# Kernel optimization log

Measured on AMD Instinct MI355X. Metric: run time of the kernel, lower is better.

The kernel has to match this reference:

```python
import jax, jax.numpy as jnp
import numpy as np

B, T, C = 2, 2048, 1024
NH, NKV, HD, NG = 16, 8, 64, 8   # heads, kv heads, head_dim, global heads
NG_KV = NG * NKV // NH           # global kv heads = 4
VE_CH = 32                       # ve_gate input channels
WIN = 1024                       # local sliding-window (left) size


def setup_inputs() -> dict:
    key = jax.random.key(0)
    ks = jax.random.split(key, 8)
    x = jax.random.normal(ks[0], (B, T, C), jnp.float32)
    ve = jax.random.normal(ks[1], (B, T, NKV * HD), jnp.float32)
    # true rotary tables over half the head dim
    half = HD // 2
    inv_freq = 1.0 / (10000.0 ** (np.arange(half, dtype=np.float64) / half))
    ang = np.arange(T, dtype=np.float64)[:, None] * inv_freq[None, :]
    cos = jnp.asarray(np.cos(ang), jnp.float32)[None, :, None, :]  # [1,T,1,32]
    sin = jnp.asarray(np.sin(ang), jnp.float32)[None, :, None, :]
    s = C ** -0.5
    Wq = jax.random.normal(ks[2], (C, NH * HD), jnp.float32) * s
    Wk = jax.random.normal(ks[3], (C, NKV * HD), jnp.float32) * s
    Wv = jax.random.normal(ks[4], (C, NKV * HD), jnp.float32) * s
    Wproj = jax.random.normal(ks[5], (C, C), jnp.float32) * s
    Wg = jax.random.normal(ks[6], (VE_CH, NKV), jnp.float32) * (VE_CH ** -0.5)
    return dict(x=x, ve=ve, cos=cos, sin=sin, Wq=Wq, Wk=Wk, Wv=Wv,
                Wproj=Wproj, Wg=Wg, window=WIN)


def _rope(x, cos, sin):
    d = x.shape[-1] // 2
    x1, x2 = x[..., :d], x[..., d:]
    return jnp.concatenate([x1 * cos + x2 * sin, -x1 * sin + x2 * cos], axis=-1)


def _rms_norm(x):
    eps = jnp.asarray(jnp.finfo(x.dtype).eps, x.dtype)
    return x * jax.lax.rsqrt(jnp.mean(x * x, axis=-1, keepdims=True) + eps)


def _gqa_attn(q, k, v, left_window):
    # q: [B,T,Hq,D]; k,v: [B,T,Hk,D]; GQA with g = Hq//Hk queries per kv head.
    b, t, hq, d = q.shape
    hk = k.shape[2]
    g = hq // hk
    qg = q.reshape(b, t, hk, g, d)
    scores = jnp.einsum('bqhgd,bkhd->bhgqk', qg, k) * (d ** -0.5)
    i = jnp.arange(t)[:, None]
    j = jnp.arange(t)[None, :]
    if left_window < 0:
        mask = j <= i                       # full causal
    else:
        mask = (j <= i) & ((i - j) <= left_window)  # causal sliding window
    scores = jnp.where(mask, scores, jnp.asarray(-1e30, scores.dtype))
    p = jax.nn.softmax(scores, axis=-1)
    out = jnp.einsum('bhgqk,bkhd->bqhgd', p, v)
    return out.reshape(b, t, hq, d)


def reference(x, ve, cos, sin, Wq, Wk, Wv, Wproj, Wg, window):
    b, t, c = x.shape
    q = (x @ Wq).reshape(b, t, NH, HD)
    k = (x @ Wk).reshape(b, t, NKV, HD)
    v = (x @ Wv).reshape(b, t, NKV, HD)
    # value-embedding gating: gate = 2*sigmoid(Linear(x[..., :32])) per kv head
    gate = 2.0 * jax.nn.sigmoid(x[..., :VE_CH] @ Wg)       # [B,T,NKV]
    v = v + gate[..., None] * ve.reshape(b, t, NKV, HD)
    # inline RoPE then RMSNorm on q and k
    q = _rms_norm(_rope(q, cos, sin))
    k = _rms_norm(_rope(k, cos, sin))
    # split global (full causal) vs local (windowed) head groups
    y_global = _gqa_attn(q[:, :, :NG], k[:, :, :NG_KV], v[:, :, :NG_KV], -1)
    y_local = _gqa_attn(q[:, :, NG:], k[:, :, NG_KV:], v[:, :, NG_KV:], window)
    y = jnp.concatenate([y_global, y_local], axis=2).reshape(b, t, c)
    return y @ Wproj
```

## Files before the change

kernel.cpp:

```cpp
#include <hip/hip_runtime.h>
#include <hip/hip_bf16.h>
#include <math.h>

typedef __bf16 bf16x8 __attribute__((ext_vector_type(8)));
typedef __bf16 bf16x4 __attribute__((ext_vector_type(4)));
typedef float  f32x4  __attribute__((ext_vector_type(4)));

#define MFMA16(a, b, c) __builtin_amdgcn_mfma_f32_16x16x32_bf16((a), (b), (c), 0, 0, 0)

__device__ __forceinline__ void gload16(const void* g, void* lds) {
    __builtin_amdgcn_global_load_lds(
        (const __attribute__((address_space(1))) uint32_t*)g,
        (__attribute__((address_space(3))) uint32_t*)lds, 16, 0, 0);
}

__global__ __launch_bounds__(256)
void prep2_kernel(const float* __restrict__ x, __bf16* __restrict__ xb,
                  const float* __restrict__ Wq, const float* __restrict__ Wk,
                  const float* __restrict__ Wv, const float* __restrict__ Wproj,
                  __bf16* __restrict__ wqkvt, __bf16* __restrict__ wprojt) {
    const int bx = blockIdx.x;
    const int tid = threadIdx.x;
    if (bx < 4096) {
        int i = bx * 256 + tid;
        float4 v = reinterpret_cast<const float4*>(x)[i];
        bf16x4 o = { (__bf16)v.x, (__bf16)v.y, (__bf16)v.z, (__bf16)v.w };
        *reinterpret_cast<bf16x4*>(xb + (size_t)i * 4) = o;
        return;
    }
    __shared__ __bf16 Ts[64 * 72];
    const int idx = bx - 4096;
    const int z = idx >> 8;
    const float* W = (z == 0) ? Wq : (z == 1) ? Wk : (z == 2) ? Wv : Wproj;
    __bf16* dst = (z == 3) ? wprojt : wqkvt;
    const int N = (z == 1 || z == 2) ? 512 : 1024;
    const int nt_off = (z == 1) ? 1024 : (z == 2) ? 1536 : 0;
    const int n0 = (idx & 15) * 64, k0 = ((idx >> 4) & 15) * 64;
    if (n0 >= N) return;
    {
        int r = tid >> 2;
        int c0 = (tid & 3) * 16;
        const float4* s4 = reinterpret_cast<const float4*>(
            W + (size_t)(k0 + r) * N + n0 + c0);
        float val[16];
        #pragma unroll
        for (int q = 0; q < 4; ++q) {
            float4 v = s4[q];
            val[q * 4 + 0] = v.x; val[q * 4 + 1] = v.y;
            val[q * 4 + 2] = v.z; val[q * 4 + 3] = v.w;
        }
        #pragma unroll
        for (int j = 0; j < 16; ++j) Ts[(c0 + j) * 72 + r] = (__bf16)val[j];
    }
    __syncthreads();
    {
        int n = tid >> 2, kg = (tid & 3) * 16;
        __bf16* out = dst + (size_t)(nt_off + n0 + n) * 1024 + k0 + kg;
        bf16x8 t0 = *reinterpret_cast<const bf16x8*>(&Ts[n * 72 + kg]);
        bf16x8 t1 = *reinterpret_cast<const bf16x8*>(&Ts[n * 72 + kg + 8]);
        *reinterpret_cast<bf16x8*>(out) = t0;
        *reinterpret_cast<bf16x8*>(out + 8) = t1;
    }
}

template <typename OutT>
__global__ __launch_bounds__(256)
void gemm_bf16(const __bf16* __restrict__ A, const __bf16* __restrict__ Bt,
               OutT* __restrict__ C, int M, int N, int K) {
    __shared__ __align__(16) __bf16 As[128 * 64];
    __shared__ __align__(16) __bf16 Bs[128 * 64];
    const int tid = threadIdx.x;
    const int lane = tid & 63, w = tid >> 6;
    const int wr = w >> 1, wc = w & 1;
    const int nwg = gridDim.x * gridDim.y;
    const int id = blockIdx.y * gridDim.x + blockIdx.x;
    const int nid = (id & 7) * (nwg >> 3) + (id >> 3);
    const int bxs = nid % gridDim.x, bys = nid / gridDim.x;
    const int bm = bys * 128, bn = bxs * 128;
    const int lhi = lane >> 4, llo = lane & 15;
    const int gsrc = (lane & 7) ^ ((lane >> 3) & 7);

    f32x4 acc[4][4] = {};

    for (int k0 = 0; k0 < K; k0 += 64) {
        __syncthreads();
        const __bf16* Ab = A + (size_t)bm * K + k0;
        const __bf16* Bb = Bt + (size_t)bn * K + k0;
        #pragma unroll
        for (int rr = 0; rr < 4; ++rr) {
            int c = rr * 4 + w;
            int r = c * 8 + (lane >> 3);
            gload16(Ab + (size_t)r * K + gsrc * 8, (char*)As + c * 1024);
            gload16(Bb + (size_t)r * K + gsrc * 8, (char*)Bs + c * 1024);
        }
        __syncthreads();

        #pragma unroll
        for (int ks = 0; ks < 2; ++ks) {
            bf16x8 af[4], bfr[4];
            int g = ks * 4 + lhi;
            #pragma unroll
            for (int i = 0; i < 4; ++i) {
                int ra = wr * 64 + i * 16 + llo;
                af[i] = *reinterpret_cast<const bf16x8*>(
                    (const char*)As + ra * 128 + ((g ^ (ra & 7)) << 4));
                int rb = wc * 64 + i * 16 + llo;
                bfr[i] = *reinterpret_cast<const bf16x8*>(
                    (const char*)Bs + rb * 128 + ((g ^ (rb & 7)) << 4));
            }
            #pragma unroll
            for (int i = 0; i < 4; ++i)
                #pragma unroll
                for (int j = 0; j < 4; ++j)
                    acc[i][j] = MFMA16(af[i], bfr[j], acc[i][j]);
        }
    }

    #pragma unroll
    for (int i = 0; i < 4; ++i) {
        #pragma unroll
        for (int j = 0; j < 4; ++j) {
            int col = bn + wc * 64 + j * 16 + llo;
            #pragma unroll
            for (int r = 0; r < 4; ++r) {
                int row = bm + wr * 64 + i * 16 + lhi * 4 + r;
                C[(size_t)row * N + col] = (OutT)acc[i][j][r];
            }
        }
    }
}

__global__ __launch_bounds__(256)
void post2_kernel(__bf16* __restrict__ qkv, const float* __restrict__ x,
                  const float* __restrict__ ve, const float* __restrict__ Wg,
                  const float* __restrict__ cosb, const float* __restrict__ sinb,
                  __bf16* __restrict__ vT) {
    const int id = blockIdx.x;
    const int tid = threadIdx.x;
    if (id < 3072) {
        const int u = id >> 7;
        const int row = (id & 127) * 32 + (tid >> 3);
        const int j = tid & 7;
        const int t = row & 2047;
        const int off = (u < 16) ? u * 64 : 1024 + (u - 16) * 64;
        __bf16* p = qkv + (size_t)row * 2048 + off + j * 8;
        bf16x8 v8 = *(const bf16x8*)p;
        float v[8], pr[8];
        #pragma unroll
        for (int e = 0; e < 8; ++e) v[e] = (float)v8[e];
        #pragma unroll
        for (int e = 0; e < 8; ++e) pr[e] = __shfl_xor(v[e], 4, 64);
        const float* cp = cosb + t * 32 + (j & 3) * 8;
        const float* sp = sinb + t * 32 + (j & 3) * 8;
        float4 c0 = *(const float4*)cp, c1 = *(const float4*)(cp + 4);
        float4 s0 = *(const float4*)sp, s1 = *(const float4*)(sp + 4);
        float cs[8] = {c0.x, c0.y, c0.z, c0.w, c1.x, c1.y, c1.z, c1.w};
        float sn[8] = {s0.x, s0.y, s0.z, s0.w, s1.x, s1.y, s1.z, s1.w};
        float r[8];
        if (j < 4) {
            #pragma unroll
            for (int e = 0; e < 8; ++e) r[e] = v[e] * cs[e] + pr[e] * sn[e];
        } else {
            #pragma unroll
            for (int e = 0; e < 8; ++e) r[e] = v[e] * cs[e] - pr[e] * sn[e];
        }
        float s = 0.f;
        #pragma unroll
        for (int e = 0; e < 8; ++e) s = fmaf(r[e], r[e], s);
        s += __shfl_xor(s, 1, 64);
        s += __shfl_xor(s, 2, 64);
        s += __shfl_xor(s, 4, 64);
        float scale = rsqrtf(s * (1.0f / 64.0f) + 1.1920929e-07f);
        if (u < 16) scale *= 0.18033688011116012f;
        bf16x8 o;
        #pragma unroll
        for (int e = 0; e < 8; ++e) o[e] = (__bf16)(r[e] * scale);
        *(bf16x8*)p = o;
    } else {
        __shared__ __bf16 Ts[64 * 72];
        const int rem = id - 3072;
        const int ch = rem & 63;
        const int h = rem >> 6;
        {
            int r = tid >> 2, c0 = (tid & 3) * 16;
            int grow = ch * 64 + r;
            float gz = 0.f;
            {
                const float* xr = x + (size_t)grow * 1024 + (tid & 3) * 8;
                #pragma unroll
                for (int i = 0; i < 8; ++i)
                    gz = fmaf(xr[i], Wg[((tid & 3) * 8 + i) * 8 + h], gz);
                gz += __shfl_xor(gz, 1, 64);
                gz += __shfl_xor(gz, 2, 64);
            }
            float g = 2.0f / (1.0f + expf(-gz));
            const __bf16* vp = qkv + (size_t)grow * 2048 + 1536 + h * 64 + c0;
            const float* vep = ve + (size_t)grow * 512 + h * 64 + c0;
            bf16x8 v0 = *reinterpret_cast<const bf16x8*>(vp);
            bf16x8 v1 = *reinterpret_cast<const bf16x8*>(vp + 8);
            #pragma unroll
            for (int j = 0; j < 8; ++j) {
                Ts[(c0 + j) * 72 + r]     = (__bf16)((float)v0[j] + g * vep[j]);
                Ts[(c0 + 8 + j) * 72 + r] = (__bf16)((float)v1[j] + g * vep[8 + j]);
            }
        }
        __syncthreads();
        {
            int d = tid >> 2, t0l = (tid & 3) * 16;
            int b = ch >> 5, tloc = (ch & 31) * 64;
            __bf16* out = vT + ((size_t)((b * 8 + h) * 64 + d)) * 2048 + tloc + t0l;
            bf16x8 t0 = *reinterpret_cast<const bf16x8*>(&Ts[d * 72 + t0l]);
            bf16x8 t1 = *reinterpret_cast<const bf16x8*>(&Ts[d * 72 + t0l + 8]);
            *reinterpret_cast<bf16x8*>(out) = t0;
            *reinterpret_cast<bf16x8*>(out + 8) = t1;
        }
    }
}

__global__ __launch_bounds__(256, 6)
void attn_mfma(const __bf16* __restrict__ qkv, const __bf16* __restrict__ vT,
               __bf16* __restrict__ y, const int* __restrict__ winp) {
    __shared__ __align__(16) __bf16 Ks[64 * 64];
    __shared__ __align__(16) __bf16 VTs[64 * 64];
    __shared__ __align__(16) __bf16 Ps[4][16 * 64];

    const int bid = blockIdx.x;
    const int kvh = bid & 7;
    int tdec = bid >> 3;
    const int b = tdec & 1; tdec >>= 1;
    const int qh = tdec & 1;
    const int qt = 31 - (tdec >> 1);
    const int h = (kvh < 4) ? (kvh * 2 + qh) : (8 + (kvh - 4) * 2 + qh);
    const int q0 = qt * 64;
    const int tid = threadIdx.x, lane = tid & 63, w = tid >> 6;
    const int lhi = lane >> 4, llo = lane & 15;
    const int gsrc = (lane & 7) ^ ((lane >> 3) & 7);
    const int win = (h < 8) ? -1 : winp[0];
    const int winv = (win < 0) ? (1 << 30) : win;

    const __bf16* kbase = qkv + (size_t)(b * 2048) * 2048 + 1024 + kvh * 64;
    const __bf16* vtbase = vT + ((size_t)((b * 8 + kvh) * 64)) * 2048;

    int kts = 0;
    if (win >= 0) { int s = q0 - win; if (s > 0) kts = s >> 6; }

    const __bf16* qrow = qkv + (size_t)(b * 2048 + q0 + w * 16 + llo) * 2048
                         + h * 64 + lhi * 8;
    bf16x8 qf[2];
    qf[0] = *(const bf16x8*)(qrow);
    qf[1] = *(const bf16x8*)(qrow + 32);

    auto STAGE = [&](int ktx) {
        #pragma unroll
        for (int rr = 0; rr < 2; ++rr) {
            int c = rr * 4 + w;
            int r = c * 8 + (lane >> 3);
            gload16(kbase + (size_t)(ktx * 64 + r) * 2048 + gsrc * 8,
                    (char*)Ks + c * 1024);
            gload16(vtbase + (size_t)r * 2048 + ktx * 64 + gsrc * 8,
                    (char*)VTs + c * 1024);
        }
    };

    f32x4 oaccT[4] = {};
    float lrow = 0.f;

    const int pswz = (llo & 7) << 4;

    for (int kt = kts; kt <= qt; ++kt) {
        STAGE(kt);
        __syncthreads();

        f32x4 sacc[4] = {};
        __builtin_amdgcn_s_setprio(1);
        #pragma unroll
        for (int ks = 0; ks < 2; ++ks) {
            #pragma unroll
            for (int kj = 0; kj < 4; ++kj) {
                int rb = kj * 16 + llo;
                bf16x8 bk = *(const bf16x8*)((const char*)&Ks[0]
                    + rb * 128 + (((ks * 4 + lhi) ^ (rb & 7)) << 4));
                sacc[kj] = MFMA16(bk, qf[ks], sacc[kj]);
            }
        }
        __builtin_amdgcn_s_setprio(0);

        const bool needMask = (kt == qt) || (win >= 0 && kt * 64 < q0 + 63 - winv);

        float sv[16];
        #pragma unroll
        for (int kj = 0; kj < 4; ++kj)
            #pragma unroll
            for (int r = 0; r < 4; ++r)
                sv[kj * 4 + r] = sacc[kj][r];
        if (needMask) {
            int qrowi = q0 + w * 16 + llo;
            #pragma unroll
            for (int kj = 0; kj < 4; ++kj)
                #pragma unroll
                for (int r = 0; r < 4; ++r) {
                    int key = kt * 64 + kj * 16 + lhi * 4 + r;
                    bool ok = (key <= qrowi) && (qrowi - key <= winv);
                    if (!ok) sv[kj * 4 + r] = -__builtin_inff();
                }
        }

        float p[16];
        #pragma unroll
        for (int t = 0; t < 16; ++t)
            p[t] = __builtin_amdgcn_exp2f(sv[t]);

        #pragma unroll
        for (int kj = 0; kj < 4; ++kj) {
            bf16x4 pk = { (__bf16)p[kj * 4 + 0], (__bf16)p[kj * 4 + 1],
                          (__bf16)p[kj * 4 + 2], (__bf16)p[kj * 4 + 3] };
            *(bf16x4*)((char*)&Ps[w][0]
                + ((llo * 128 + kj * 32 + lhi * 8) ^ pswz)) = pk;
        }

        #pragma unroll
        for (int st = 8; st >= 1; st >>= 1)
            #pragma unroll
            for (int t = 0; t < st; ++t) p[t] += p[t + st];
        lrow += p[0];

        __builtin_amdgcn_s_setprio(1);
        #pragma unroll
        for (int ks = 0; ks < 2; ++ks) {
            bf16x8 ap = *(const bf16x8*)((const char*)&Ps[w][0]
                + ((llo * 128 + ks * 64 + lhi * 16) ^ pswz));
            #pragma unroll
            for (int dj = 0; dj < 4; ++dj) {
                int rv = dj * 16 + llo;
                bf16x8 bv = *(const bf16x8*)((const char*)&VTs[0]
                    + rv * 128 + (((ks * 4 + lhi) ^ (rv & 7)) << 4));
                oaccT[dj] = MFMA16(bv, ap, oaccT[dj]);
            }
        }
        __builtin_amdgcn_s_setprio(0);

        __syncthreads();
    }

    lrow += __shfl_xor(lrow, 16, 64);
    lrow += __shfl_xor(lrow, 32, 64);

    float inv = 1.0f / lrow;
    int row = b * 2048 + q0 + w * 16 + llo;
    #pragma unroll
    for (int dj = 0; dj < 4; ++dj) {
        bf16x4 o = { (__bf16)(oaccT[dj][0] * inv), (__bf16)(oaccT[dj][1] * inv),
                     (__bf16)(oaccT[dj][2] * inv), (__bf16)(oaccT[dj][3] * inv) };
        *(bf16x4*)(&y[(size_t)row * 1024 + h * 64 + dj * 16 + lhi * 4]) = o;
    }
}

extern "C" void kernel_launch(void* const* d_in, const int* in_sizes, int n_in,
                              void* d_out, int out_size, void* d_ws, size_t ws_size,
                              hipStream_t stream) {
    const float* x     = (const float*)d_in[0];
    const float* ve    = (const float*)d_in[1];
    const float* cosb  = (const float*)d_in[2];
    const float* sinb  = (const float*)d_in[3];
    const float* Wq    = (const float*)d_in[4];
    const float* Wk    = (const float*)d_in[5];
    const float* Wv    = (const float*)d_in[6];
    const float* Wproj = (const float*)d_in[7];
    const float* Wg    = (const float*)d_in[8];
    const int*   winp  = (const int*)d_in[9];

    char* ws = (char*)d_ws;
    __bf16* qkv    = (__bf16*)(ws);
    __bf16* vT     = (__bf16*)(ws + (16u << 20));
    __bf16* ybuf   = (__bf16*)(ws + (20u << 20));
    __bf16* xb     = (__bf16*)(ws + (28u << 20));
    __bf16* wqkvt  = (__bf16*)(ws + (36u << 20));
    __bf16* wprojt = (__bf16*)(ws + (40u << 20));

    prep2_kernel<<<5120, 256, 0, stream>>>(x, xb, Wq, Wk, Wv, Wproj, wqkvt, wprojt);
    gemm_bf16<__bf16><<<dim3(16, 32), 256, 0, stream>>>(xb, wqkvt, qkv, 4096, 2048, 1024);
    post2_kernel<<<3584, 256, 0, stream>>>(qkv, x, ve, Wg, cosb, sinb, vT);
    attn_mfma<<<1024, 256, 0, stream>>>(qkv, vT, ybuf, winp);
    gemm_bf16<float><<<dim3(8, 32), 256, 0, stream>>>(ybuf, wprojt, (float*)d_out, 4096, 1024, 1024);
}
```

Measured before the change: 104.9 us.

## Restructure attention into single-wave blocks handling 32 query rows

The attention kernel changes from 256-thread blocks (4 waves x 16 query rows per 64-row tile) to 64-thread single-wave blocks that each process 32 query rows across two MFMA row tiles, using a 2048-block grid. Each wave loads the full K/V tile itself and reuses the K and V fragments across both row tiles, which roughly halves the LDS staging traffic per query row. It also gives finer causal work granularity, since the last key tile now ends at a 32-row boundary. In exchange each wave does all of the tile loading, and the __syncthreads barriers now cover only one wave. Occupancy changes from 6x256-thread to 2x64-thread launch bounds, which may reduce latency hiding.

```diff
diff --git a/kernel.cpp b/kernel.cpp
--- a/kernel.cpp
+++ b/kernel.cpp
@@ -217,22 +217,23 @@
     }
 }
 
-__global__ __launch_bounds__(256, 6)
+__global__ __launch_bounds__(64, 2)
 void attn_mfma(const __bf16* __restrict__ qkv, const __bf16* __restrict__ vT,
                __bf16* __restrict__ y, const int* __restrict__ winp) {
     __shared__ __align__(16) __bf16 Ks[64 * 64];
     __shared__ __align__(16) __bf16 VTs[64 * 64];
-    __shared__ __align__(16) __bf16 Ps[4][16 * 64];
+    __shared__ __align__(16) __bf16 Ps[32 * 64];
 
     const int bid = blockIdx.x;
     const int kvh = bid & 7;
-    int tdec = bid >> 3;
-    const int b = tdec & 1; tdec >>= 1;
-    const int qh = tdec & 1;
-    const int qt = 31 - (tdec >> 1);
+    const int rest = bid >> 3;
+    const int qh = rest & 1;
+    const int u = rest >> 1;
+    const int b = u & 1;
+    const int qt32 = 63 - (u >> 1);
     const int h = (kvh < 4) ? (kvh * 2 + qh) : (8 + (kvh - 4) * 2 + qh);
-    const int q0 = qt * 64;
-    const int tid = threadIdx.x, lane = tid & 63, w = tid >> 6;
+    const int q0 = qt32 * 32;
+    const int lane = threadIdx.x;
     const int lhi = lane >> 4, llo = lane & 15;
     const int gsrc = (lane & 7) ^ ((lane >> 3) & 7);
     const int win = (h < 8) ? -1 : winp[0];
@@ -243,98 +244,107 @@
 
     int kts = 0;
     if (win >= 0) { int s = q0 - win; if (s > 0) kts = s >> 6; }
-
-    const __bf16* qrow = qkv + (size_t)(b * 2048 + q0 + w * 16 + llo) * 2048
+    const int ktlast = (q0 + 31) >> 6;
+
+    const __bf16* qrow = qkv + (size_t)(b * 2048 + q0 + llo) * 2048
                          + h * 64 + lhi * 8;
-    bf16x8 qf[2];
-    qf[0] = *(const bf16x8*)(qrow);
-    qf[1] = *(const bf16x8*)(qrow + 32);
-
-    auto STAGE = [&](int ktx) {
-        #pragma unroll
-        for (int rr = 0; rr < 2; ++rr) {
-            int c = rr * 4 + w;
-            int r = c * 8 + (lane >> 3);
-            gload16(kbase + (size_t)(ktx * 64 + r) * 2048 + gsrc * 8,
-                    (char*)Ks + c * 1024);
-            gload16(vtbase + (size_t)r * 2048 + ktx * 64 + gsrc * 8,
-                    (char*)VTs + c * 1024);
-        }
-    };
-
-    f32x4 oaccT[4] = {};
-    float lrow = 0.f;
-
+    bf16x8 qf[2][2];
+    qf[0][0] = *(const bf16x8*)(qrow);
+    qf[0][1] = *(const bf16x8*)(qrow + 32);
+    qf[1][0] = *(const bf16x8*)(qrow + 16 * 2048);
+    qf[1][1] = *(const bf16x8*)(qrow + 16 * 2048 + 32);
+
+    f32x4 oaccT[2][4] = {};
+    float lrow[2] = {0.f, 0.f};
     const int pswz = (llo & 7) << 4;
 
-    for (int kt = kts; kt <= qt; ++kt) {
-        STAGE(kt);
+    for (int kt = kts; kt <= ktlast; ++kt) {
+        #pragma unroll
+        for (int i = 0; i < 8; ++i) {
+            int r = i * 8 + (lane >> 3);
+            gload16(kbase + (size_t)(kt * 64 + r) * 2048 + gsrc * 8,
+                    (char*)Ks + i * 1024);
+            gload16(vtbase + (size_t)r * 2048 + kt * 64 + gsrc * 8,
+                    (char*)VTs + i * 1024);
+        }
         __syncthreads();
 
-        f32x4 sacc[4] = {};
+        bf16x8 bk[4][2];
+        #pragma unroll
+        for (int kj = 0; kj < 4; ++kj) {
+            int rb = kj * 16 + llo;
+            #pragma unroll
+            for (int ks = 0; ks < 2; ++ks)
+                bk[kj][ks] = *(const bf16x8*)((const char*)&Ks[0]
+                    + rb * 128 + (((ks * 4 + lhi) ^ (rb & 7)) << 4));
+        }
+        f32x4 sacc[2][4] = {};
         __builtin_amdgcn_s_setprio(1);
         #pragma unroll
+        for (int ks = 0; ks < 2; ++ks)
+            #pragma unroll
+            for (int mi = 0; mi < 2; ++mi)
+                #pragma unroll
+                for (int kj = 0; kj < 4; ++kj)
+                    sacc[mi][kj] = MFMA16(bk[kj][ks], qf[mi][ks], sacc[mi][kj]);
+        __builtin_amdgcn_s_setprio(0);
+
+        const bool needMask = (kt == ktlast) ||
+                              (win >= 0 && kt * 64 < q0 + 31 - winv);
+
+        #pragma unroll
+        for (int mi = 0; mi < 2; ++mi) {
+            float sv[16];
+            #pragma unroll
+            for (int kj = 0; kj < 4; ++kj)
+                #pragma unroll
+                for (int r = 0; r < 4; ++r)
+                    sv[kj * 4 + r] = sacc[mi][kj][r];
+            if (needMask) {
+                int qrowi = q0 + mi * 16 + llo;
+                #pragma unroll
+                for (int kj = 0; kj < 4; ++kj)
+                    #pragma unroll
+                    for (int r = 0; r < 4; ++r) {
+                        int key = kt * 64 + kj * 16 + lhi * 4 + r;
+                        bool ok = (key <= qrowi) && (qrowi - key <= winv);
+                        if (!ok) sv[kj * 4 + r] = -__builtin_inff();
+                    }
+            }
+            float p[16];
+            #pragma unroll
+            for (int t = 0; t < 16; ++t)
+                p[t] = __builtin_amdgcn_exp2f(sv[t]);
+            #pragma unroll
+            for (int kj = 0; kj < 4; ++kj) {
+                bf16x4 pk = { (__bf16)p[kj * 4 + 0], (__bf16)p[kj * 4 + 1],
+                              (__bf16)p[kj * 4 + 2], (__bf16)p[kj * 4 + 3] };
+                *(bf16x4*)((char*)&Ps[0]
+                    + (((mi * 16 + llo) * 128 + kj * 32 + lhi * 8) ^ pswz)) = pk;
+            }
+            #pragma unroll
+            for (int st = 8; st >= 1; st >>= 1)
+                #pragma unroll
+                for (int t = 0; t < st; ++t) p[t] += p[t + st];
+            lrow[mi] += p[0];
+        }
+
+        __builtin_amdgcn_s_setprio(1);
+        #pragma unroll
         for (int ks = 0; ks < 2; ++ks) {
-            #pragma unroll
-            for (int kj = 0; kj < 4; ++kj) {
-                int rb = kj * 16 + llo;
-                bf16x8 bk = *(const bf16x8*)((const char*)&Ks[0]
-                    + rb * 128 + (((ks * 4 + lhi) ^ (rb & 7)) << 4));
-                sacc[kj] = MFMA16(bk, qf[ks], sacc[kj]);
-            }
-        }
-        __builtin_amdgcn_s_setprio(0);
-
-        const bool needMask = (kt == qt) || (win >= 0 && kt * 64 < q0 + 63 - winv);
-
-        float sv[16];
-        #pragma unroll
-        for (int kj = 0; kj < 4; ++kj)
-            #pragma unroll
-            for (int r = 0; r < 4; ++r)
-                sv[kj * 4 + r] = sacc[kj][r];
-        if (needMask) {
-            int qrowi = q0 + w * 16 + llo;
-            #pragma unroll
-            for (int kj = 0; kj < 4; ++kj)
-                #pragma unroll
-                for (int r = 0; r < 4; ++r) {
-                    int key = kt * 64 + kj * 16 + lhi * 4 + r;
-                    bool ok = (key <= qrowi) && (qrowi - key <= winv);
-                    if (!ok) sv[kj * 4 + r] = -__builtin_inff();
-                }
-        }
-
-        float p[16];
-        #pragma unroll
-        for (int t = 0; t < 16; ++t)
-            p[t] = __builtin_amdgcn_exp2f(sv[t]);
-
-        #pragma unroll
-        for (int kj = 0; kj < 4; ++kj) {
-            bf16x4 pk = { (__bf16)p[kj * 4 + 0], (__bf16)p[kj * 4 + 1],
-                          (__bf16)p[kj * 4 + 2], (__bf16)p[kj * 4 + 3] };
-            *(bf16x4*)((char*)&Ps[w][0]
-                + ((llo * 128 + kj * 32 + lhi * 8) ^ pswz)) = pk;
-        }
-
-        #pragma unroll
-        for (int st = 8; st >= 1; st >>= 1)
-            #pragma unroll
-            for (int t = 0; t < st; ++t) p[t] += p[t + st];
-        lrow += p[0];
-
-        __builtin_amdgcn_s_setprio(1);
-        #pragma unroll
-        for (int ks = 0; ks < 2; ++ks) {
-            bf16x8 ap = *(const bf16x8*)((const char*)&Ps[w][0]
-                + ((llo * 128 + ks * 64 + lhi * 16) ^ pswz));
+            bf16x8 ap[2];
+            #pragma unroll
+            for (int mi = 0; mi < 2; ++mi)
+                ap[mi] = *(const bf16x8*)((const char*)&Ps[0]
+                    + (((mi * 16 + llo) * 128 + ks * 64 + lhi * 16) ^ pswz));
             #pragma unroll
             for (int dj = 0; dj < 4; ++dj) {
                 int rv = dj * 16 + llo;
                 bf16x8 bv = *(const bf16x8*)((const char*)&VTs[0]
                     + rv * 128 + (((ks * 4 + lhi) ^ (rv & 7)) << 4));
-                oaccT[dj] = MFMA16(bv, ap, oaccT[dj]);
+                #pragma unroll
+                for (int mi = 0; mi < 2; ++mi)
+                    oaccT[mi][dj] = MFMA16(bv, ap[mi], oaccT[mi][dj]);
             }
         }
         __builtin_amdgcn_s_setprio(0);
@@ -342,16 +352,24 @@
         __syncthreads();
     }
 
-    lrow += __shfl_xor(lrow, 16, 64);
-    lrow += __shfl_xor(lrow, 32, 64);
-
-    float inv = 1.0f / lrow;
-    int row = b * 2048 + q0 + w * 16 + llo;
     #pragma unroll
-    for (int dj = 0; dj < 4; ++dj) {
-        bf16x4 o = { (__bf16)(oaccT[dj][0] * inv), (__bf16)(oaccT[dj][1] * inv),
-                     (__bf16)(oaccT[dj][2] * inv), (__bf16)(oaccT[dj][3] * inv) };
-        *(bf16x4*)(&y[(size_t)row * 1024 + h * 64 + dj * 16 + lhi * 4]) = o;
+    for (int mi = 0; mi < 2; ++mi) {
+        lrow[mi] += __shfl_xor(lrow[mi], 16, 64);
+        lrow[mi] += __shfl_xor(lrow[mi], 32, 64);
+    }
+
+    #pragma unroll
+    for (int mi = 0; mi < 2; ++mi) {
+        float inv = 1.0f / lrow[mi];
+        int row = b * 2048 + q0 + mi * 16 + llo;
+        #pragma unroll
+        for (int dj = 0; dj < 4; ++dj) {
+            bf16x4 o = { (__bf16)(oaccT[mi][dj][0] * inv),
+                         (__bf16)(oaccT[mi][dj][1] * inv),
+                         (__bf16)(oaccT[mi][dj][2] * inv),
+                         (__bf16)(oaccT[mi][dj][3] * inv) };
+            *(bf16x4*)(&y[(size_t)row * 1024 + h * 64 + dj * 16 + lhi * 4]) = o;
+        }
     }
 }
 
@@ -380,6 +398,6 @@
     prep2_kernel<<<5120, 256, 0, stream>>>(x, xb, Wq, Wk, Wv, Wproj, wqkvt, wprojt);
     gemm_bf16<__bf16><<<dim3(16, 32), 256, 0, stream>>>(xb, wqkvt, qkv, 4096, 2048, 1024);
     post2_kernel<<<3584, 256, 0, stream>>>(qkv, x, ve, Wg, cosb, sinb, vT);
-    attn_mfma<<<1024, 256, 0, stream>>>(qkv, vT, ybuf, winp);
+    attn_mfma<<<2048, 64, 0, stream>>>(qkv, vT, ybuf, winp);
     gemm_bf16<float><<<dim3(8, 32), 256, 0, stream>>>(ybuf, wprojt, (float*)d_out, 4096, 1024, 1024);
 }
```

Result: slower. 115.3 us (+9.9%).
